# Performance work log

Measured on AMD Instinct MI355X. Metric: run time of the kernel, lower is better.

The kernel has to match this reference:

```python
import jax, jax.numpy as jnp
import numpy as np

B, N, D = 8, 8192, 256
H, DK, M, DH = 8, 32, 64, 512   # heads, per-head key dim, n_omega random features, mlp hidden
DV = D // H                      # per-head value dim
EPS = 1e-3                       # keras LayerNormalization default epsilon


def _layer_norm(x, g, b):
    mu = jnp.mean(x, axis=-1, keepdims=True)
    var = jnp.var(x, axis=-1, keepdims=True)
    return g * (x - mu) * jax.lax.rsqrt(var + EPS) + b


def _phi(x, omega):
    # Performer positive random features. x: (B,H,N,DK), omega: (DK,M)
    x = x / (DK ** 0.25)
    proj = jnp.einsum('bhnd,dm->bhnm', x, omega)
    sq = 0.5 * jnp.sum(x * x, axis=-1, keepdims=True)
    return jnp.exp(proj - sq) / jnp.sqrt(jnp.asarray(M, x.dtype))


def _mhla(x, Wq, bq, Wk, bk, Wv, bv, Wo, bo, omega):
    # x: (B,N,D). Multi-head linear (kernelized) attention.
    q = (x @ Wq + bq).reshape(B, N, H, DK).transpose(0, 2, 1, 3)  # bhnd
    k = (x @ Wk + bk).reshape(B, N, H, DK).transpose(0, 2, 1, 3)
    v = (x @ Wv + bv).reshape(B, N, H, DV).transpose(0, 2, 1, 3)
    pq = _phi(q, omega)                                   # (B,H,N,M)
    pk = _phi(k, omega)                                   # (B,H,N,M)
    kv = jnp.einsum('bhnm,bhnd->bhmd', pk, v)             # (B,H,M,DV)
    num = jnp.einsum('bhnm,bhmd->bhnd', pq, kv)           # (B,H,N,DV)
    den = jnp.einsum('bhnm,bhm->bhn', pq, jnp.sum(pk, axis=2))
    out = num / den[..., None]
    out = out.transpose(0, 2, 1, 3).reshape(B, N, D)
    return out @ Wo + bo


def _gru_gate(x, y, Wr, Ur, Wz, Uz, Wg, Ug, bg):
    # GTrXL gating: x = residual (old state), y = new sublayer output.
    r = jax.nn.sigmoid(y @ Wr + x @ Ur)
    z = jax.nn.sigmoid(y @ Wz + x @ Uz - bg)
    h = jnp.tanh(y @ Wg + (r * x) @ Ug)
    return (1.0 - z) * x + z * h


def setup_inputs() -> dict:
    key = jax.random.key(0)
    ks = iter(jax.random.split(key, 40))
    w = lambda *s: jax.random.normal(next(ks), s, jnp.float32) * 0.02
    inp = {
        'x': jax.random.normal(next(ks), (B, N, D), jnp.float32),
        'ln1_g': jnp.ones((D,), jnp.float32), 'ln1_b': jnp.zeros((D,), jnp.float32),
        'Wq': w(D, H * DK), 'bq': jnp.zeros((H * DK,), jnp.float32),
        'Wk': w(D, H * DK), 'bk': jnp.zeros((H * DK,), jnp.float32),
        'Wv': w(D, H * DV), 'bv': jnp.zeros((H * DV,), jnp.float32),
        'Wo': w(D, D), 'bo': jnp.zeros((D,), jnp.float32),
        'omega': jax.random.normal(next(ks), (DK, M), jnp.float32),
        'g1_Wr': w(D, D), 'g1_Ur': w(D, D), 'g1_Wz': w(D, D), 'g1_Uz': w(D, D),
        'g1_Wg': w(D, D), 'g1_Ug': w(D, D), 'g1_bg': 2.0 * jnp.ones((D,), jnp.float32),
        'ln2_g': jnp.ones((D,), jnp.float32), 'ln2_b': jnp.zeros((D,), jnp.float32),
        'W1': w(D, DH), 'b1': jnp.zeros((DH,), jnp.float32),
        'W2': w(DH, D), 'b2': jnp.zeros((D,), jnp.float32),
        'g2_Wr': w(D, D), 'g2_Ur': w(D, D), 'g2_Wz': w(D, D), 'g2_Uz': w(D, D),
        'g2_Wg': w(D, D), 'g2_Ug': w(D, D), 'g2_bg': 2.0 * jnp.ones((D,), jnp.float32),
    }
    return inp


def reference(x, ln1_g, ln1_b, Wq, bq, Wk, bk, Wv, bv, Wo, bo, omega,
              g1_Wr, g1_Ur, g1_Wz, g1_Uz, g1_Wg, g1_Ug, g1_bg,
              ln2_g, ln2_b, W1, b1, W2, b2,
              g2_Wr, g2_Ur, g2_Wz, g2_Uz, g2_Wg, g2_Ug, g2_bg):
    residual = x
    h = _layer_norm(x, ln1_g, ln1_b)
    h = _mhla(h, Wq, bq, Wk, bk, Wv, bv, Wo, bo, omega)
    h = _gru_gate(residual, h, g1_Wr, g1_Ur, g1_Wz, g1_Uz, g1_Wg, g1_Ug, g1_bg)
    residual = h
    h2 = _layer_norm(h, ln2_g, ln2_b)
    h2 = jax.nn.relu(h2 @ W1 + b1)
    h2 = jax.nn.relu(h2 @ W2 + b2)
    out = _gru_gate(residual, h2, g2_Wr, g2_Ur, g2_Wz, g2_Uz, g2_Wg, g2_Ug, g2_bg)
    return out
```

## Files before the change

kernel.cpp:

```cpp
#include <hip/hip_runtime.h>

#define B_ 8
#define N_ 8192
#define H_ 8
#define KSPLIT 16
#define BN 65536

typedef float f32x4 __attribute__((ext_vector_type(4)));
typedef __bf16 bf16x8 __attribute__((ext_vector_type(8)));
typedef unsigned short u16;

__device__ __forceinline__ u16 f2b(float f) {
  union { float f; unsigned u; } v; v.f = f;
  return (u16)((v.u + 0x7fffu + ((v.u >> 16) & 1u)) >> 16);
}
__device__ __forceinline__ float b2f(u16 u) {
  union { unsigned u; float f; } v; v.u = ((unsigned)u) << 16;
  return v.f;
}

__device__ __forceinline__ void gload16(const void* g, const void* lds) {
  __builtin_amdgcn_global_load_lds(
      (const __attribute__((address_space(1))) unsigned int*)(unsigned long long)g,
      (__attribute__((address_space(3))) unsigned int*)(unsigned long long)lds,
      16, 0, 0);
}

__device__ __forceinline__ void ld16f(const float* p, float* f) {
#pragma unroll
  for (int j = 0; j < 4; ++j) {
    float4 q = *(const float4*)(p + j * 4);
    f[j * 4 + 0] = q.x; f[j * 4 + 1] = q.y; f[j * 4 + 2] = q.z; f[j * 4 + 3] = q.w;
  }
}
__device__ __forceinline__ void ld16b(const u16* p, float* f) {
  uint4 a = *(const uint4*)p, b = *(const uint4*)(p + 8);
  const unsigned uu[8] = {a.x, a.y, a.z, a.w, b.x, b.y, b.z, b.w};
#pragma unroll
  for (int j = 0; j < 8; ++j) {
    f[2 * j]     = b2f((u16)(uu[j] & 0xffff));
    f[2 * j + 1] = b2f((u16)(uu[j] >> 16));
  }
}
__device__ __forceinline__ void st16b(u16* p, const float* f) {
  u16 o[16];
#pragma unroll
  for (int j = 0; j < 16; ++j) o[j] = f2b(f[j]);
  *(uint4*)p = *(const uint4*)o;
  *(uint4*)(p + 8) = *(const uint4*)(o + 8);
}
__device__ __forceinline__ void st16f(float* p, const float* f) {
#pragma unroll
  for (int j = 0; j < 4; ++j) {
    float4 q; q.x = f[j * 4]; q.y = f[j * 4 + 1]; q.z = f[j * 4 + 2]; q.w = f[j * 4 + 3];
    *(float4*)(p + j * 4) = q;
  }
}

template <int MODE, int XBF, int CF32, int BSEL>
__global__ __launch_bounds__(512) void gemm2(
    const u16* __restrict__ A1, int lda1, const u16* __restrict__ A2, int lda2,
    const u16* __restrict__ BT, int ldb,
    const float* __restrict__ bias, const void* __restrict__ auxX,
    const u16* __restrict__ auxZ, const float* __restrict__ auxS,
    void* __restrict__ Cv, void* __restrict__ Cv2, void* __restrict__ Cv3,
    int ldc, int K) {
  __shared__ __align__(16) u16 As[3][4096];
  __shared__ __align__(16) u16 Bs[3][8192];
  const int t = threadIdx.x, lane = t & 63, w = t >> 6;
  const int nwg = gridDim.x * gridDim.y;
  const int flat = blockIdx.x + gridDim.x * blockIdx.y;
  const int wg = (flat & 7) * (nwg >> 3) + (flat >> 3);
  const int bx = wg % gridDim.x, by = wg / gridDim.x;
  const int rowBase = by * 128, colBase = bx * 256;
  const u16* BTb = BSEL ? BT + (size_t)(by >> 6) * 131072 : BT;

  const int lr = lane & 15, kg = lane >> 4;
  const int wrow = (w >> 2) * 64, wcol = (w & 3) * 64;

  f32x4 acc[4][4];
#pragma unroll
  for (int m = 0; m < 4; ++m)
#pragma unroll
    for (int n = 0; n < 4; ++n) acc[m][n] = 0.f;

  const int nt = K >> 5;
  auto stage = [&](int s) {
    const int buf = s % 3;
    const int k0 = s << 5;
    const u16* Ap; int la, ka;
    if (k0 < 256) { Ap = A1; la = lda1; ka = k0; }
    else          { Ap = A2; la = lda2; ka = k0 - 256; }
    {
      int row = t >> 2, sl = t & 3;
      int ks = (sl ^ ((row & 6) >> 1)) * 8;
      gload16(&Ap[(size_t)(rowBase + row) * la + ka + ks], &As[buf][t * 8]);
    }
#pragma unroll
    for (int j = 0; j < 2; ++j) {
      int slot = j * 512 + t;
      int col = slot >> 2, sl = slot & 3;
      int ks = (sl ^ ((col & 6) >> 1)) * 8;
      gload16(&BTb[(size_t)(colBase + col) * ldb + k0 + ks], &Bs[buf][slot * 8]);
    }
  };

  auto lbar = [&]() {
    asm volatile("s_waitcnt lgkmcnt(0)" ::: "memory");
    __builtin_amdgcn_sched_barrier(0);
    __builtin_amdgcn_s_barrier();
    __builtin_amdgcn_sched_barrier(0);
  };

  stage(0);
  stage(1);
  for (int s = 0; s < nt; ++s) {
    const int buf = s % 3;
    if (nt - s > 1) asm volatile("s_waitcnt vmcnt(3)" ::: "memory");
    else            asm volatile("s_waitcnt vmcnt(0)" ::: "memory");
    __builtin_amdgcn_sched_barrier(0);
    __builtin_amdgcn_s_barrier();
    __builtin_amdgcn_sched_barrier(0);
    if (s + 2 < nt) stage(s + 2);
    bf16x8 af[4], bf[4];
#pragma unroll
    for (int m = 0; m < 4; ++m) {
      int row = wrow + m * 16 + lr;
      af[m] = *(const bf16x8*)&As[buf][row * 32 + (kg ^ ((row & 6) >> 1)) * 8];
    }
#pragma unroll
    for (int n = 0; n < 4; ++n) {
      int col = wcol + n * 16 + lr;
      bf[n] = *(const bf16x8*)&Bs[buf][col * 32 + (kg ^ ((col & 6) >> 1)) * 8];
    }
    __builtin_amdgcn_s_setprio(1);
#pragma unroll
    for (int m = 0; m < 4; ++m)
#pragma unroll
      for (int n = 0; n < 4; ++n)
        acc[m][n] = __builtin_amdgcn_mfma_f32_16x16x32_bf16(af[m], bf[n], acc[m][n], 0, 0, 0);
    __builtin_amdgcn_s_setprio(0);
  }

  lbar();
  float* scr = (float*)&Bs[0][0];
#pragma unroll
  for (int m = 0; m < 4; ++m) {
    if (m) lbar();
#pragma unroll
    for (int n = 0; n < 4; ++n)
#pragma unroll
      for (int i = 0; i < 4; ++i)
        scr[((w >> 2) * 16 + kg * 4 + i) * 260 + wcol + n * 16 + lr] = acc[m][n][i];
    lbar();
    const int sr = t >> 4, cs = (t & 15) * 16;
    const int grow = rowBase + (sr >> 4) * 64 + m * 16 + (sr & 15);
    const int gcol = colBase + cs;
    float vv[16];
#pragma unroll
    for (int j = 0; j < 4; ++j) {
      float4 q = *(const float4*)&scr[sr * 260 + cs + j * 4];
      vv[j * 4] = q.x; vv[j * 4 + 1] = q.y; vv[j * 4 + 2] = q.z; vv[j * 4 + 3] = q.w;
    }
    if (MODE == 0 || MODE == 1) {
      float bb[16]; ld16f(&bias[gcol], bb);
#pragma unroll
      for (int j = 0; j < 16; ++j) {
        vv[j] += bb[j];
        if (MODE == 1) vv[j] = fmaxf(vv[j], 0.f);
      }
      st16b(&((u16*)Cv)[(size_t)grow * ldc + gcol], vv);
    } else if (MODE == 5) {
      float sx = auxS[(size_t)grow * 8 + (gcol >> 6)];
#pragma unroll
      for (int j = 0; j < 16; ++j) vv[j] = __expf(vv[j] - sx) * 0.125f;
      st16b(&((u16*)Cv)[(size_t)grow * ldc + gcol], vv);
    } else if (MODE == 6) {
      float sx = auxS[(size_t)grow * 8 + (gcol >> 5)];
#pragma unroll
      for (int j = 0; j < 16; ++j) vv[j] *= sx;
      st16b(&((u16*)Cv)[(size_t)grow * ldc + gcol], vv);
    } else if (MODE == 7) {
      float bb[16]; ld16f(&bias[gcol], bb);
#pragma unroll
      for (int j = 0; j < 16; ++j) vv[j] += bb[j];
      u16* Cp; int c2;
      if (colBase < 256)      { Cp = (u16*)Cv;  c2 = gcol; }
      else if (colBase < 512) { Cp = (u16*)Cv2; c2 = gcol - 256; }
      else                    { Cp = (u16*)Cv3; c2 = gcol - 512; }
      st16b(&Cp[(size_t)grow * ldc + c2], vv);
    } else if (MODE == 8) {
      if (colBase < 256) {
        float xv[16];
        if (XBF) ld16b(&((const u16*)auxX)[(size_t)grow * 256 + gcol], xv);
        else     ld16f(&((const float*)auxX)[(size_t)grow * 256 + gcol], xv);
#pragma unroll
        for (int j = 0; j < 16; ++j) vv[j] = (1.f / (1.f + __expf(-vv[j]))) * xv[j];
        st16b(&((u16*)Cv)[(size_t)grow * ldc + gcol], vv);
      } else {
        float bb[16]; ld16f(&bias[gcol - 256], bb);
#pragma unroll
        for (int j = 0; j < 16; ++j) vv[j] = 1.f / (1.f + __expf(-(vv[j] - bb[j])));
        st16b(&((u16*)Cv2)[(size_t)grow * ldc + gcol - 256], vv);
      }
    } else if (MODE == 4) {
      float zz[16], xv[16];
      ld16b(&auxZ[(size_t)grow * 256 + gcol], zz);
      if (XBF) ld16b(&((const u16*)auxX)[(size_t)grow * 256 + gcol], xv);
      else     ld16f(&((const float*)auxX)[(size_t)grow * 256 + gcol], xv);
#pragma unroll
      for (int j = 0; j < 16; ++j)
        vv[j] = (1.f - zz[j]) * xv[j] + zz[j] * tanhf(vv[j]);
      if (CF32) st16f(&((float*)Cv)[(size_t)grow * ldc + gcol], vv);
      else      st16b(&((u16*)Cv)[(size_t)grow * ldc + gcol], vv);
    }
  }
}

__global__ __launch_bounds__(256) void fkv_kernel(const u16* __restrict__ Kb,
                                                  const u16* __restrict__ Vb,
                                                  const u16* __restrict__ omT,
                                                  float* __restrict__ part) {
  __shared__ __align__(16) char smem[33792];
  u16* Ks  = (u16*)smem;
  u16* omS = Ks + 4096;
  u16* pkT = omS + 2048;
  u16* vT  = pkT + 64 * 72;
  float* sqL = (float*)(vT + 48 * 72);
  float* red = (float*)smem;

  const int bh = blockIdx.x, split = blockIdx.y;
  const int b = bh >> 3, h = bh & 7;
  const int t = threadIdx.x, lane = t & 63, w = t >> 6;
  const int lr = lane & 15, kg = lane >> 4;
  const size_t rbase = (size_t)b * N_ + (size_t)split * (N_ / KSPLIT);

  {
    int m = t >> 2, sl = t & 3;
    gload16(&omT[m * 32 + ((sl ^ ((m & 6) >> 1)) * 8)], &omS[t * 8]);
  }
  for (int i = t; i < 16 * 128; i += 256) {
    int r = 32 + (i >> 7), tok = i & 127;
    vT[r * 72 + tok] = (r == 32) ? (u16)0x3f80 : (u16)0;
  }

  f32x4 kacc[4][3];
#pragma unroll
  for (int mi = 0; mi < 4; ++mi)
#pragma unroll
    for (int ni = 0; ni < 3; ++ni) kacc[mi][ni] = 0.f;

  for (int tile = 0; tile < (N_ / KSPLIT) / 128; ++tile) {
    __syncthreads();
    const size_t gt0 = rbase + tile * 128;
#pragma unroll
    for (int j = 0; j < 2; ++j) {
      int slot = j * 256 + t;
      int tok = slot >> 2, sl = slot & 3;
      gload16(&Kb[(gt0 + tok) * 256 + h * 32 + ((sl ^ ((tok & 6) >> 1)) * 8)],
              &Ks[slot * 8]);
    }
#pragma unroll
    for (int j = 0; j < 2; ++j) {
      int slot = j * 256 + t;
      int tok = slot >> 2, seg = slot & 3;
      uint4 q = *(const uint4*)&Vb[(gt0 + tok) * 256 + h * 32 + seg * 8];
      const unsigned uu[4] = {q.x, q.y, q.z, q.w};
#pragma unroll
      for (int jj = 0; jj < 4; ++jj) {
        vT[(seg * 8 + jj * 2 + 0) * 72 + tok] = (u16)(uu[jj] & 0xffffu);
        vT[(seg * 8 + jj * 2 + 1) * 72 + tok] = (u16)(uu[jj] >> 16);
      }
    }
    asm volatile("s_waitcnt vmcnt(0)" ::: "memory");
    __syncthreads();

    uint4 araw[2];
    bf16x8 af[2];
#pragma unroll
    for (int mi = 0; mi < 2; ++mi) {
      int row = w * 32 + mi * 16 + lr;
      araw[mi] = *(const uint4*)&Ks[row * 32 + (kg ^ ((row & 6) >> 1)) * 8];
      af[mi] = *(const bf16x8*)&araw[mi];
    }
#pragma unroll
    for (int mi = 0; mi < 2; ++mi) {
      const unsigned uu[4] = {araw[mi].x, araw[mi].y, araw[mi].z, araw[mi].w};
      float s = 0.f;
#pragma unroll
      for (int j = 0; j < 4; ++j) {
        float lo = b2f((u16)(uu[j] & 0xffffu)), hi = b2f((u16)(uu[j] >> 16));
        s = __fmaf_rn(lo, lo, s); s = __fmaf_rn(hi, hi, s);
      }
      s += __shfl_xor(s, 16);
      s += __shfl_xor(s, 32);
      if (lane < 16) sqL[w * 32 + mi * 16 + lr] = 0.0883883476483184f * s;
    }
    bf16x8 bo[4];
#pragma unroll
    for (int ni = 0; ni < 4; ++ni) {
      int col = ni * 16 + lr;
      bo[ni] = *(const bf16x8*)&omS[col * 32 + (kg ^ ((col & 6) >> 1)) * 8];
    }
    f32x4 pacc[2][4];
#pragma unroll
    for (int mi = 0; mi < 2; ++mi)
#pragma unroll
      for (int ni = 0; ni < 4; ++ni) {
        f32x4 z = 0.f;
        pacc[mi][ni] = __builtin_amdgcn_mfma_f32_16x16x32_bf16(af[mi], bo[ni], z, 0, 0, 0);
      }
    float sqv[2][4];
#pragma unroll
    for (int mi = 0; mi < 2; ++mi)
#pragma unroll
      for (int i = 0; i < 4; ++i)
        sqv[mi][i] = sqL[w * 32 + mi * 16 + kg * 4 + i];
#pragma unroll
    for (int mi = 0; mi < 2; ++mi)
#pragma unroll
      for (int ni = 0; ni < 4; ++ni) {
        u16 p4[4];
#pragma unroll
        for (int i = 0; i < 4; ++i)
          p4[i] = f2b(__expf(pacc[mi][ni][i] - sqv[mi][i]) * 0.125f);
        int m = ni * 16 + lr;
        int tok = w * 32 + mi * 16 + kg * 4;
        *(unsigned long long*)&pkT[m * 72 + tok] = *(const unsigned long long*)p4;
      }
    __syncthreads();

    {
      int ktok = w * 32;
      bf16x8 a2[4], b2v[3];
#pragma unroll
      for (int mi = 0; mi < 4; ++mi)
        a2[mi] = *(const bf16x8*)&pkT[(mi * 16 + lr) * 72 + ktok + kg * 8];
#pragma unroll
      for (int ni = 0; ni < 3; ++ni)
        b2v[ni] = *(const bf16x8*)&vT[(ni * 16 + lr) * 72 + ktok + kg * 8];
#pragma unroll
      for (int mi = 0; mi < 4; ++mi)
#pragma unroll
        for (int ni = 0; ni < 3; ++ni)
          kacc[mi][ni] = __builtin_amdgcn_mfma_f32_16x16x32_bf16(a2[mi], b2v[ni], kacc[mi][ni], 0, 0, 0);
    }
  }

  __syncthreads();
#pragma unroll
  for (int mi = 0; mi < 4; ++mi) {
#pragma unroll
    for (int ni = 0; ni < 3; ++ni) {
      if (ni < 2) {
#pragma unroll
        for (int i = 0; i < 4; ++i)
          red[w * 2112 + (mi * 16 + kg * 4 + i) * 33 + ni * 16 + lr] = kacc[mi][ni][i];
      } else if (lr == 0) {
#pragma unroll
        for (int i = 0; i < 4; ++i)
          red[w * 2112 + (mi * 16 + kg * 4 + i) * 33 + 32] = kacc[mi][2][i];
      }
    }
  }
  __syncthreads();
  float* dst = part + (size_t)(bh * KSPLIT + split) * 2112;
  for (int idx = t; idx < 2112; idx += 256) {
    int m, c;
    if (idx < 2048) { m = idx >> 5; c = idx & 31; }
    else            { m = idx - 2048; c = 32; }
    float s = 0.f;
#pragma unroll
    for (int w4 = 0; w4 < 4; ++w4) s += red[w4 * 2112 + m * 33 + c];
    dst[idx] = s;
  }
}

struct TJob { const float* s; u16* d; int lds, ldd, rows, cols; };
struct TJobs { TJob j[18]; };
__global__ __launch_bounds__(256) void wt_kernel(TJobs J) {
  TJob jb = J.j[blockIdx.y];
  int ntc = jb.cols >> 6;
  int tile = blockIdx.x;
  if (tile >= (jb.rows >> 6) * ntc) return;
  int tr = (tile / ntc) << 6, tc = (tile % ntc) << 6;
  __shared__ float sm[64][68];
  int t = threadIdx.x;
#pragma unroll
  for (int i = 0; i < 4; ++i) {
    int idx = t + 256 * i;
    int r = idx >> 4, c = (idx & 15) * 4;
    float4 v = *(const float4*)&jb.s[(size_t)(tr + r) * jb.lds + tc + c];
    sm[r][c] = v.x; sm[r][c + 1] = v.y; sm[r][c + 2] = v.z; sm[r][c + 3] = v.w;
  }
  __syncthreads();
#pragma unroll
  for (int i = 0; i < 4; ++i) {
    int idx = t + 256 * i;
    int c = idx >> 4, r = (idx & 15) * 4;
    ushort4 p; p.x = f2b(sm[r][c]); p.y = f2b(sm[r + 1][c]);
    p.z = f2b(sm[r + 2][c]); p.w = f2b(sm[r + 3][c]);
    *(ushort4*)&jb.d[(size_t)(tc + c) * jb.ldd + tr + r] = p;
  }
}

__global__ __launch_bounds__(256) void wphiT_kernel(const float* __restrict__ omega,
                                                    u16* __restrict__ w) {
  int idx = blockIdx.x * 256 + threadIdx.x;
  int c = idx >> 8, k = idx & 255;
  float v = 0.f;
  if ((k >> 5) == (c >> 6)) v = omega[(k & 31) * 64 + (c & 63)] * 0.4204482076268573f;
  w[idx] = f2b(v);
}

__global__ __launch_bounds__(256) void omT_kernel(const float* __restrict__ omega,
                                                  u16* __restrict__ o) {
  int idx = blockIdx.x * 256 + threadIdx.x;
  int m = idx >> 5, k = idx & 31;
  o[idx] = f2b(omega[k * 64 + m] * 0.4204482076268573f);
}

__global__ __launch_bounds__(256) void bias_kernel(const float* bk, const float* bv,
                                                   const float* bq, float* dst) {
  int t = threadIdx.x;
  dst[t] = bk[t]; dst[256 + t] = bv[t]; dst[512 + t] = bq[t];
}

__global__ __launch_bounds__(256) void kvbdT_kernel(const float* __restrict__ kvfin,
                                                    u16* __restrict__ kb) {
  int idx = blockIdx.x * 256 + threadIdx.x;
  int b = idx >> 17, rem = idx & 131071;
  int c = rem >> 9, k = rem & 511;
  float v = 0.f;
  if ((k >> 6) == (c >> 5))
    v = kvfin[(size_t)(b * 8 + (k >> 6)) * 2112 + (k & 63) * 32 + (c & 31)];
  kb[idx] = f2b(v);
}

__global__ __launch_bounds__(256) void cvtb_kernel(const float* __restrict__ x,
                                                   u16* __restrict__ o) {
  size_t i = ((size_t)blockIdx.x * 256 + threadIdx.x) * 16;
  float f[16];
  ld16f(&x[i], f);
  st16b(&o[i], f);
}

template <int XBF>
__global__ __launch_bounds__(256) void ln_kernel2(const void* __restrict__ xv,
                                                  const float* __restrict__ g,
                                                  const float* __restrict__ b,
                                                  u16* __restrict__ out) {
  const int row = blockIdx.x * 4 + (threadIdx.x >> 6);
  const int lane = threadIdx.x & 63;
  float v[4];
  if (XBF) {
    uint2 u = *(const uint2*)&((const u16*)xv)[(size_t)row * 256 + lane * 4];
    v[0] = b2f((u16)(u.x & 0xffff)); v[1] = b2f((u16)(u.x >> 16));
    v[2] = b2f((u16)(u.y & 0xffff)); v[3] = b2f((u16)(u.y >> 16));
  } else {
    float4 f = *(const float4*)&((const float*)xv)[(size_t)row * 256 + lane * 4];
    v[0] = f.x; v[1] = f.y; v[2] = f.z; v[3] = f.w;
  }
  float s = v[0] + v[1] + v[2] + v[3];
  float s2 = v[0] * v[0] + v[1] * v[1] + v[2] * v[2] + v[3] * v[3];
#pragma unroll
  for (int off = 1; off < 64; off <<= 1) {
    s += __shfl_xor(s, off);
    s2 += __shfl_xor(s2, off);
  }
  const float mu = s * (1.f / 256.f);
  const float var = s2 * (1.f / 256.f) - mu * mu;
  const float rs = rsqrtf(var + 1e-3f);
  const float4 gv = *(const float4*)&g[lane * 4];
  const float4 bv = *(const float4*)&b[lane * 4];
  ushort4 o;
  o.x = f2b(gv.x * (v[0] - mu) * rs + bv.x);
  o.y = f2b(gv.y * (v[1] - mu) * rs + bv.y);
  o.z = f2b(gv.z * (v[2] - mu) * rs + bv.z);
  o.w = f2b(gv.w * (v[3] - mu) * rs + bv.w);
  *(ushort4*)&out[(size_t)row * 256 + lane * 4] = o;
}

__global__ __launch_bounds__(256) void sqh_kernel2(const u16* __restrict__ X,
                                                   float* __restrict__ sq) {
  const int row = blockIdx.x * 4 + (threadIdx.x >> 6);
  const int lane = threadIdx.x & 63;
  uint2 u = *(const uint2*)&X[(size_t)row * 256 + lane * 4];
  float a = b2f((u16)(u.x & 0xffff)), bb = b2f((u16)(u.x >> 16));
  float c = b2f((u16)(u.y & 0xffff)), d = b2f((u16)(u.y >> 16));
  float s = a * a + bb * bb + c * c + d * d;
  s += __shfl_xor(s, 1); s += __shfl_xor(s, 2); s += __shfl_xor(s, 4);
  if ((lane & 7) == 0) sq[(size_t)row * 8 + (lane >> 3)] = 0.0883883476483184f * s;
}

__global__ __launch_bounds__(256) void kv_reduce_kernel(const float* __restrict__ part,
                                                        float* __restrict__ fin) {
  const int bh = blockIdx.x, t = threadIdx.x;
  for (int idx = t; idx < 2112; idx += 256) {
    float s = 0.f;
#pragma unroll
    for (int sp = 0; sp < KSPLIT; ++sp) s += part[(size_t)(bh * KSPLIT + sp) * 2112 + idx];
    fin[(size_t)bh * 2112 + idx] = s;
  }
}

__global__ __launch_bounds__(256) void den_kernel(const u16* __restrict__ pq,
                                                  const float* __restrict__ kvfin,
                                                  float* __restrict__ rden) {
  const int row = blockIdx.x * 4 + (threadIdx.x >> 6);
  const int lane = threadIdx.x & 63;
  const int h = lane >> 3, m0 = (lane & 7) * 8;
  const int b = row >> 13;
  const float* s = &kvfin[(size_t)(b * 8 + h) * 2112 + 2048 + m0];
  uint4 pv = *(const uint4*)&pq[(size_t)row * 512 + h * 64 + m0];
  const unsigned uu[4] = {pv.x, pv.y, pv.z, pv.w};
  float acc = 0.f;
#pragma unroll
  for (int j = 0; j < 4; ++j) {
    union { unsigned u; float f; } lo, hi;
    lo.u = uu[j] << 16; hi.u = uu[j] & 0xffff0000u;
    acc = __fmaf_rn(lo.f, s[2 * j], acc);
    acc = __fmaf_rn(hi.f, s[2 * j + 1], acc);
  }
  acc += __shfl_xor(acc, 1); acc += __shfl_xor(acc, 2); acc += __shfl_xor(acc, 4);
  if ((lane & 7) == 0) rden[(size_t)row * 8 + h] = 1.0f / acc;
}

extern "C" void kernel_launch(void* const* d_in, const int* in_sizes, int n_in,
                              void* d_out, int out_size, void* d_ws, size_t ws_size,
                              hipStream_t stream) {
  (void)in_sizes; (void)n_in; (void)out_size; (void)ws_size;
  const float* x     = (const float*)d_in[0];
  const float* ln1_g = (const float*)d_in[1];
  const float* ln1_b = (const float*)d_in[2];
  const float* Wq    = (const float*)d_in[3];
  const float* bq    = (const float*)d_in[4];
  const float* Wk    = (const float*)d_in[5];
  const float* bk    = (const float*)d_in[6];
  const float* Wv    = (const float*)d_in[7];
  const float* bv    = (const float*)d_in[8];
  const float* Wo    = (const float*)d_in[9];
  const float* bo    = (const float*)d_in[10];
  const float* omega = (const float*)d_in[11];
  const float* g1_Wr = (const float*)d_in[12];
  const float* g1_Ur = (const float*)d_in[13];
  const float* g1_Wz = (const float*)d_in[14];
  const float* g1_Uz = (const float*)d_in[15];
  const float* g1_Wg = (const float*)d_in[16];
  const float* g1_Ug = (const float*)d_in[17];
  const float* g1_bg = (const float*)d_in[18];
  const float* ln2_g = (const float*)d_in[19];
  const float* ln2_b = (const float*)d_in[20];
  const float* W1    = (const float*)d_in[21];
  const float* b1    = (const float*)d_in[22];
  const float* W2    = (const float*)d_in[23];
  const float* b2    = (const float*)d_in[24];
  const float* g2_Wr = (const float*)d_in[25];
  const float* g2_Ur = (const float*)d_in[26];
  const float* g2_Wz = (const float*)d_in[27];
  const float* g2_Uz = (const float*)d_in[28];
  const float* g2_Wg = (const float*)d_in[29];
  const float* g2_Ug = (const float*)d_in[30];
  const float* g2_bg = (const float*)d_in[31];

  const size_t SZB = (size_t)BN * 256;
  u16* S0 = (u16*)d_ws;
  u16* S1 = S0 + SZB;
  u16* S2 = S1 + SZB;
  u16* S3 = S2 + SZB;
  u16* qkvT  = S3 + SZB;
  u16* wphiT = qkvT + 768 * 256;
  u16* woT   = wphiT + 512 * 256;
  u16* g1rzT = woT + 65536;
  u16* g1hpT = g1rzT + 262144;
  u16* w1T   = g1hpT + 131072;
  u16* w2T   = w1T + 131072;
  u16* g2rzT = w2T + 131072;
  u16* g2hpT = g2rzT + 262144;
  u16* kvbdT = g2hpT + 131072;
  u16* omTg  = kvbdT + 1048576;
  float* bias768 = (float*)(omTg + 2048);
  float* kvpart  = bias768 + 768;
  float* kvfin   = kvpart + (size_t)64 * KSPLIT * 2112;
  float* sq      = kvfin + 64 * 2112;
  u16* db = (u16*)d_out;
  u16* xb = db + SZB;
  float* outf = (float*)d_out;

  dim3 blk(256), blkG(512);
  dim3 g1c(1, BN / 128), g2c(2, BN / 128), g3c(3, BN / 128);

  TJobs J;
  auto job = [](const float* s, u16* d, int lds, int ldd, int r, int c) {
    TJob t; t.s = s; t.d = d; t.lds = lds; t.ldd = ldd; t.rows = r; t.cols = c; return t;
  };
  J.j[0]  = job(Wk, qkvT, 256, 256, 256, 256);
  J.j[1]  = job(Wv, qkvT + 256 * 256, 256, 256, 256, 256);
  J.j[2]  = job(Wq, qkvT + 512 * 256, 256, 256, 256, 256);
  J.j[3]  = job(Wo, woT, 256, 256, 256, 256);
  J.j[4]  = job(g1_Wr, g1rzT, 256, 512, 256, 256);
  J.j[5]  = job(g1_Ur, g1rzT + 256, 256, 512, 256, 256);
  J.j[6]  = job(g1_Wz, g1rzT + 256 * 512, 256, 512, 256, 256);
  J.j[7]  = job(g1_Uz, g1rzT + 256 * 512 + 256, 256, 512, 256, 256);
  J.j[8]  = job(g1_Wg, g1hpT, 256, 512, 256, 256);
  J.j[9]  = job(g1_Ug, g1hpT + 256, 256, 512, 256, 256);
  J.j[10] = job(W1, w1T, 512, 256, 256, 512);
  J.j[11] = job(W2, w2T, 256, 512, 512, 256);
  J.j[12] = job(g2_Wr, g2rzT, 256, 512, 256, 256);
  J.j[13] = job(g2_Ur, g2rzT + 256, 256, 512, 256, 256);
  J.j[14] = job(g2_Wz, g2rzT + 256 * 512, 256, 512, 256, 256);
  J.j[15] = job(g2_Uz, g2rzT + 256 * 512 + 256, 256, 512, 256, 256);
  J.j[16] = job(g2_Wg, g2hpT, 256, 512, 256, 256);
  J.j[17] = job(g2_Ug, g2hpT + 256, 256, 512, 256, 256);
  wt_kernel<<<dim3(32, 18), blk, 0, stream>>>(J);
  wphiT_kernel<<<512, blk, 0, stream>>>(omega, wphiT);
  omT_kernel<<<8, blk, 0, stream>>>(omega, omTg);
  bias_kernel<<<1, blk, 0, stream>>>(bk, bv, bq, bias768);

  ln_kernel2<0><<<BN / 4, blk, 0, stream>>>(x, ln1_g, ln1_b, S0);
  gemm2<7,0,0,0><<<g3c, blkG, 0, stream>>>(S0, 256, S0, 256, qkvT, 256,
      bias768, nullptr, nullptr, nullptr, S1, S2, S3, 256, 256);
  fkv_kernel<<<dim3(64, KSPLIT), blk, 0, stream>>>(S1, S2, omTg, kvpart);
  kv_reduce_kernel<<<64, blk, 0, stream>>>(kvpart, kvfin);
  kvbdT_kernel<<<4096, blk, 0, stream>>>(kvfin, kvbdT);
  sqh_kernel2<<<BN / 4, blk, 0, stream>>>(S3, sq);
  gemm2<5,0,0,0><<<g2c, blkG, 0, stream>>>(S3, 256, S3, 256, wphiT, 256,
      nullptr, nullptr, nullptr, sq, db, nullptr, nullptr, 512, 256);
  den_kernel<<<BN / 4, blk, 0, stream>>>(db, kvfin, sq);
  gemm2<6,0,0,1><<<g1c, blkG, 0, stream>>>(db, 512, db + 256, 512, kvbdT, 512,
      nullptr, nullptr, nullptr, sq, S3, nullptr, nullptr, 256, 512);
  gemm2<0,0,0,0><<<g1c, blkG, 0, stream>>>(S3, 256, S3, 256, woT, 256,
      bo, nullptr, nullptr, nullptr, db, nullptr, nullptr, 256, 256);
  cvtb_kernel<<<BN / 16, blk, 0, stream>>>(x, xb);
  gemm2<8,0,0,0><<<g2c, blkG, 0, stream>>>(db, 256, xb, 256, g1rzT, 512,
      g1_bg, x, nullptr, nullptr, S1, S2, nullptr, 256, 512);
  gemm2<4,0,0,0><<<g1c, blkG, 0, stream>>>(db, 256, S1, 256, g1hpT, 512,
      nullptr, x, S2, nullptr, S3, nullptr, nullptr, 256, 512);
  ln_kernel2<1><<<BN / 4, blk, 0, stream>>>(S3, ln2_g, ln2_b, S0);
  gemm2<1,0,0,0><<<g2c, blkG, 0, stream>>>(S0, 256, S0, 256, w1T, 256,
      b1, nullptr, nullptr, nullptr, db, nullptr, nullptr, 512, 256);
  gemm2<1,0,0,0><<<g1c, blkG, 0, stream>>>(db, 512, db + 256, 512, w2T, 512,
      b2, nullptr, nullptr, nullptr, S1, nullptr, nullptr, 256, 512);
  gemm2<8,1,0,0><<<g2c, blkG, 0, stream>>>(S1, 256, S3, 256, g2rzT, 512,
      g2_bg, S3, nullptr, nullptr, S2, S0, nullptr, 256, 512);
  gemm2<4,1,1,0><<<g1c, blkG, 0, stream>>>(S1, 256, S2, 256, g2hpT, 512,
      nullptr, S3, S0, nullptr, outf, nullptr, nullptr, 256, 512);
}
```

Measured before the change: 625.6 us.

## Enlarge GEMM row tile to 256 and deepen LDS pipeline to four stages

```diff
diff --git a/kernel.cpp b/kernel.cpp
--- a/kernel.cpp
+++ b/kernel.cpp
@@ -65,43 +65,45 @@
     const u16* __restrict__ auxZ, const float* __restrict__ auxS,
     void* __restrict__ Cv, void* __restrict__ Cv2, void* __restrict__ Cv3,
     int ldc, int K) {
-  __shared__ __align__(16) u16 As[3][4096];
-  __shared__ __align__(16) u16 Bs[3][8192];
+  __shared__ __align__(16) u16 As[4][8192];
+  __shared__ __align__(16) u16 Bs[4][8192];
   const int t = threadIdx.x, lane = t & 63, w = t >> 6;
   const int nwg = gridDim.x * gridDim.y;
   const int flat = blockIdx.x + gridDim.x * blockIdx.y;
   const int wg = (flat & 7) * (nwg >> 3) + (flat >> 3);
   const int bx = wg % gridDim.x, by = wg / gridDim.x;
-  const int rowBase = by * 128, colBase = bx * 256;
-  const u16* BTb = BSEL ? BT + (size_t)(by >> 6) * 131072 : BT;
+  const int rowBase = by * 256, colBase = bx * 256;
+  const u16* BTb = BSEL ? BT + (size_t)(rowBase >> 13) * 131072 : BT;
 
   const int lr = lane & 15, kg = lane >> 4;
-  const int wrow = (w >> 2) * 64, wcol = (w & 3) * 64;
-
-  f32x4 acc[4][4];
-#pragma unroll
-  for (int m = 0; m < 4; ++m)
+  const int wrow = (w >> 2) * 128, wcol = (w & 3) * 64;
+
+  f32x4 acc[8][4];
+#pragma unroll
+  for (int m = 0; m < 8; ++m)
 #pragma unroll
     for (int n = 0; n < 4; ++n) acc[m][n] = 0.f;
 
   const int nt = K >> 5;
   auto stage = [&](int s) {
-    const int buf = s % 3;
+    const int buf = s & 3;
     const int k0 = s << 5;
     const u16* Ap; int la, ka;
     if (k0 < 256) { Ap = A1; la = lda1; ka = k0; }
     else          { Ap = A2; la = lda2; ka = k0 - 256; }
-    {
-      int row = t >> 2, sl = t & 3;
+#pragma unroll
+    for (int j = 0; j < 2; ++j) {
+      int g = j * 512 + t;
+      int row = g >> 2, sl = g & 3;
       int ks = (sl ^ ((row & 6) >> 1)) * 8;
-      gload16(&Ap[(size_t)(rowBase + row) * la + ka + ks], &As[buf][t * 8]);
+      gload16(&Ap[(size_t)(rowBase + row) * la + ka + ks], &As[buf][g * 8]);
     }
 #pragma unroll
     for (int j = 0; j < 2; ++j) {
-      int slot = j * 512 + t;
-      int col = slot >> 2, sl = slot & 3;
+      int g = j * 512 + t;
+      int col = g >> 2, sl = g & 3;
       int ks = (sl ^ ((col & 6) >> 1)) * 8;
-      gload16(&BTb[(size_t)(colBase + col) * ldb + k0 + ks], &Bs[buf][slot * 8]);
+      gload16(&BTb[(size_t)(colBase + col) * ldb + k0 + ks], &Bs[buf][g * 8]);
     }
   };
 
@@ -114,17 +116,20 @@
 
   stage(0);
   stage(1);
+  stage(2);
   for (int s = 0; s < nt; ++s) {
-    const int buf = s % 3;
-    if (nt - s > 1) asm volatile("s_waitcnt vmcnt(3)" ::: "memory");
-    else            asm volatile("s_waitcnt vmcnt(0)" ::: "memory");
+    const int buf = s & 3;
+    const int rem = nt - 1 - s;
+    if (rem >= 2)      asm volatile("s_waitcnt vmcnt(8)" ::: "memory");
+    else if (rem == 1) asm volatile("s_waitcnt vmcnt(4)" ::: "memory");
+    else               asm volatile("s_waitcnt vmcnt(0)" ::: "memory");
     __builtin_amdgcn_sched_barrier(0);
     __builtin_amdgcn_s_barrier();
     __builtin_amdgcn_sched_barrier(0);
-    if (s + 2 < nt) stage(s + 2);
-    bf16x8 af[4], bf[4];
-#pragma unroll
-    for (int m = 0; m < 4; ++m) {
+    if (s + 3 < nt) stage(s + 3);
+    bf16x8 af[8], bf[4];
+#pragma unroll
+    for (int m = 0; m < 8; ++m) {
       int row = wrow + m * 16 + lr;
       af[m] = *(const bf16x8*)&As[buf][row * 32 + (kg ^ ((row & 6) >> 1)) * 8];
     }
@@ -135,7 +140,7 @@
     }
     __builtin_amdgcn_s_setprio(1);
 #pragma unroll
-    for (int m = 0; m < 4; ++m)
+    for (int m = 0; m < 8; ++m)
 #pragma unroll
       for (int n = 0; n < 4; ++n)
         acc[m][n] = __builtin_amdgcn_mfma_f32_16x16x32_bf16(af[m], bf[n], acc[m][n], 0, 0, 0);
@@ -143,18 +148,18 @@
   }
 
   lbar();
-  float* scr = (float*)&Bs[0][0];
-#pragma unroll
-  for (int m = 0; m < 4; ++m) {
-    if (m) lbar();
+  float* scr = (float*)&As[0][0];
+#pragma unroll
+  for (int mf = 0; mf < 8; ++mf) {
+    if (mf) lbar();
 #pragma unroll
     for (int n = 0; n < 4; ++n)
 #pragma unroll
       for (int i = 0; i < 4; ++i)
-        scr[((w >> 2) * 16 + kg * 4 + i) * 260 + wcol + n * 16 + lr] = acc[m][n][i];
+        scr[((w >> 2) * 16 + kg * 4 + i) * 260 + wcol + n * 16 + lr] = acc[mf][n][i];
     lbar();
     const int sr = t >> 4, cs = (t & 15) * 16;
-    const int grow = rowBase + (sr >> 4) * 64 + m * 16 + (sr & 15);
+    const int grow = rowBase + (sr >> 4) * 128 + mf * 16 + (sr & 15);
     const int gcol = colBase + cs;
     float vv[16];
 #pragma unroll
@@ -588,7 +593,7 @@
   float* outf = (float*)d_out;
 
   dim3 blk(256), blkG(512);
-  dim3 g1c(1, BN / 128), g2c(2, BN / 128), g3c(3, BN / 128);
+  dim3 g1c(1, BN / 256), g2c(2, BN / 256), g3c(3, BN / 256);
 
   TJobs J;
   auto job = [](const float* s, u16* d, int lds, int ldd, int r, int c) {
```

Measured after the change: 808.4 us. 29.2% more time.

## Fold Wo into per-batch KV matrix and fuse sq, denominator, LayerNorm into GEMM epilogues

Applied to the files above, without the earlier changes.

```diff
diff --git a/kernel.cpp b/kernel.cpp
--- a/kernel.cpp
+++ b/kernel.cpp
@@ -73,7 +73,10 @@
   const int wg = (flat & 7) * (nwg >> 3) + (flat >> 3);
   const int bx = wg % gridDim.x, by = wg / gridDim.x;
   const int rowBase = by * 128, colBase = bx * 256;
-  const u16* BTb = BSEL ? BT + (size_t)(by >> 6) * 131072 : BT;
+  const int aBase = (BSEL == 2) ? (rowBase & 255) : rowBase;
+  const u16* BTb = BT;
+  if (BSEL == 1) BTb = BT + (size_t)(rowBase >> 13) * 131072;
+  if (BSEL == 2) BTb = BT + (size_t)(rowBase >> 8) * 131072;
 
   const int lr = lane & 15, kg = lane >> 4;
   const int wrow = (w >> 2) * 64, wcol = (w & 3) * 64;
@@ -94,7 +97,7 @@
     {
       int row = t >> 2, sl = t & 3;
       int ks = (sl ^ ((row & 6) >> 1)) * 8;
-      gload16(&Ap[(size_t)(rowBase + row) * la + ka + ks], &As[buf][t * 8]);
+      gload16(&Ap[(size_t)(aBase + row) * la + ka + ks], &As[buf][t * 8]);
     }
 #pragma unroll
     for (int j = 0; j < 2; ++j) {
@@ -175,11 +178,6 @@
 #pragma unroll
       for (int j = 0; j < 16; ++j) vv[j] = __expf(vv[j] - sx) * 0.125f;
       st16b(&((u16*)Cv)[(size_t)grow * ldc + gcol], vv);
-    } else if (MODE == 6) {
-      float sx = auxS[(size_t)grow * 8 + (gcol >> 5)];
-#pragma unroll
-      for (int j = 0; j < 16; ++j) vv[j] *= sx;
-      st16b(&((u16*)Cv)[(size_t)grow * ldc + gcol], vv);
     } else if (MODE == 7) {
       float bb[16]; ld16f(&bias[gcol], bb);
 #pragma unroll
@@ -189,6 +187,15 @@
       else if (colBase < 512) { Cp = (u16*)Cv2; c2 = gcol - 256; }
       else                    { Cp = (u16*)Cv3; c2 = gcol - 512; }
       st16b(&Cp[(size_t)grow * ldc + c2], vv);
+      if (colBase == 512) {
+        float s = 0.f;
+#pragma unroll
+        for (int j = 0; j < 16; ++j) s += vv[j] * vv[j];
+        s += __shfl_xor(s, 1);
+        if ((t & 1) == 0)
+          const_cast<float*>(auxS)[(size_t)grow * 8 + ((gcol - 512) >> 5)] =
+              0.0883883476483184f * s;
+      }
     } else if (MODE == 8) {
       if (colBase < 256) {
         float xv[16];
@@ -213,6 +220,31 @@
         vv[j] = (1.f - zz[j]) * xv[j] + zz[j] * tanhf(vv[j]);
       if (CF32) st16f(&((float*)Cv)[(size_t)grow * ldc + gcol], vv);
       else      st16b(&((u16*)Cv)[(size_t)grow * ldc + gcol], vv);
+    } else if (MODE == 9) {
+      float zz[16], xv[16];
+      ld16b(&auxZ[(size_t)grow * 256 + gcol], zz);
+      ld16b(&((const u16*)auxX)[(size_t)grow * 256 + gcol], xv);
+#pragma unroll
+      for (int j = 0; j < 16; ++j)
+        vv[j] = (1.f - zz[j]) * xv[j] + zz[j] * tanhf(vv[j]);
+      st16b(&((u16*)Cv)[(size_t)grow * 256 + gcol], vv);
+      float s1 = 0.f, s2 = 0.f;
+#pragma unroll
+      for (int j = 0; j < 16; ++j) { s1 += vv[j]; s2 += vv[j] * vv[j]; }
+#pragma unroll
+      for (int off = 1; off < 16; off <<= 1) {
+        s1 += __shfl_xor(s1, off);
+        s2 += __shfl_xor(s2, off);
+      }
+      float mu = s1 * (1.f / 256.f);
+      float var = s2 * (1.f / 256.f) - mu * mu;
+      float rs = rsqrtf(var + 1e-3f);
+      float gg[16], bb2[16];
+      ld16f(&bias[gcol], gg);
+      ld16f(&auxS[gcol], bb2);
+#pragma unroll
+      for (int j = 0; j < 16; ++j) vv[j] = gg[j] * (vv[j] - mu) * rs + bb2[j];
+      st16b(&((u16*)Cv2)[(size_t)grow * 256 + gcol], vv);
     }
   }
 }
@@ -424,16 +456,17 @@
                                                    const float* bq, float* dst) {
   int t = threadIdx.x;
   dst[t] = bk[t]; dst[256 + t] = bv[t]; dst[512 + t] = bq[t];
-}
-
-__global__ __launch_bounds__(256) void kvbdT_kernel(const float* __restrict__ kvfin,
+  dst[768 + t] = 0.f; dst[1024 + t] = 0.f;
+}
+
+__global__ __launch_bounds__(256) void kvbdA_kernel(const float* __restrict__ kvfin,
                                                     u16* __restrict__ kb) {
   int idx = blockIdx.x * 256 + threadIdx.x;
   int b = idx >> 17, rem = idx & 131071;
-  int c = rem >> 9, k = rem & 511;
+  int kp = rem >> 8, d = rem & 255;
   float v = 0.f;
-  if ((k >> 6) == (c >> 5))
-    v = kvfin[(size_t)(b * 8 + (k >> 6)) * 2112 + (k & 63) * 32 + (c & 31)];
+  if ((kp >> 6) == (d >> 5))
+    v = kvfin[(size_t)(b * 8 + (kp >> 6)) * 2112 + (kp & 63) * 32 + (d & 31)];
   kb[idx] = f2b(v);
 }
 
@@ -481,18 +514,6 @@
   *(ushort4*)&out[(size_t)row * 256 + lane * 4] = o;
 }
 
-__global__ __launch_bounds__(256) void sqh_kernel2(const u16* __restrict__ X,
-                                                   float* __restrict__ sq) {
-  const int row = blockIdx.x * 4 + (threadIdx.x >> 6);
-  const int lane = threadIdx.x & 63;
-  uint2 u = *(const uint2*)&X[(size_t)row * 256 + lane * 4];
-  float a = b2f((u16)(u.x & 0xffff)), bb = b2f((u16)(u.x >> 16));
-  float c = b2f((u16)(u.y & 0xffff)), d = b2f((u16)(u.y >> 16));
-  float s = a * a + bb * bb + c * c + d * d;
-  s += __shfl_xor(s, 1); s += __shfl_xor(s, 2); s += __shfl_xor(s, 4);
-  if ((lane & 7) == 0) sq[(size_t)row * 8 + (lane >> 3)] = 0.0883883476483184f * s;
-}
-
 __global__ __launch_bounds__(256) void kv_reduce_kernel(const float* __restrict__ part,
                                                         float* __restrict__ fin) {
   const int bh = blockIdx.x, t = threadIdx.x;
@@ -504,26 +525,31 @@
   }
 }
 
-__global__ __launch_bounds__(256) void den_kernel(const u16* __restrict__ pq,
-                                                  const float* __restrict__ kvfin,
-                                                  float* __restrict__ rden) {
+__global__ __launch_bounds__(256) void den2_kernel(u16* __restrict__ pq,
+                                                   const float* __restrict__ kvfin) {
   const int row = blockIdx.x * 4 + (threadIdx.x >> 6);
   const int lane = threadIdx.x & 63;
   const int h = lane >> 3, m0 = (lane & 7) * 8;
   const int b = row >> 13;
   const float* s = &kvfin[(size_t)(b * 8 + h) * 2112 + 2048 + m0];
-  uint4 pv = *(const uint4*)&pq[(size_t)row * 512 + h * 64 + m0];
+  u16* pp = &pq[(size_t)row * 512 + h * 64 + m0];
+  uint4 pv = *(const uint4*)pp;
   const unsigned uu[4] = {pv.x, pv.y, pv.z, pv.w};
+  float vals[8];
   float acc = 0.f;
 #pragma unroll
   for (int j = 0; j < 4; ++j) {
-    union { unsigned u; float f; } lo, hi;
-    lo.u = uu[j] << 16; hi.u = uu[j] & 0xffff0000u;
-    acc = __fmaf_rn(lo.f, s[2 * j], acc);
-    acc = __fmaf_rn(hi.f, s[2 * j + 1], acc);
+    vals[2 * j]     = b2f((u16)(uu[j] & 0xffffu));
+    vals[2 * j + 1] = b2f((u16)(uu[j] >> 16));
+    acc = __fmaf_rn(vals[2 * j], s[2 * j], acc);
+    acc = __fmaf_rn(vals[2 * j + 1], s[2 * j + 1], acc);
   }
   acc += __shfl_xor(acc, 1); acc += __shfl_xor(acc, 2); acc += __shfl_xor(acc, 4);
-  if ((lane & 7) == 0) rden[(size_t)row * 8 + h] = 1.0f / acc;
+  const float r = 1.0f / acc;
+  u16 o[8];
+#pragma unroll
+  for (int j = 0; j < 8; ++j) o[j] = f2b(vals[j] * r);
+  *(uint4*)pp = *(const uint4*)o;
 }
 
 extern "C" void kernel_launch(void* const* d_in, const int* in_sizes, int n_in,
@@ -577,14 +603,15 @@
   u16* w2T   = w1T + 131072;
   u16* g2rzT = w2T + 131072;
   u16* g2hpT = g2rzT + 262144;
-  u16* kvbdT = g2hpT + 131072;
-  u16* omTg  = kvbdT + 1048576;
+  u16* kvbdA = g2hpT + 131072;
+  u16* WoKVT = kvbdA + 1048576;
+  u16* omTg  = WoKVT + 1048576;
   float* bias768 = (float*)(omTg + 2048);
-  float* kvpart  = bias768 + 768;
+  float* zero512 = bias768 + 768;
+  float* kvpart  = bias768 + 1280;
   float* kvfin   = kvpart + (size_t)64 * KSPLIT * 2112;
-  float* sq      = kvfin + 64 * 2112;
+  float* sqQ     = kvfin + 64 * 2112;
   u16* db = (u16*)d_out;
-  u16* xb = db + SZB;
   float* outf = (float*)d_out;
 
   dim3 blk(256), blkG(512);
@@ -619,24 +646,22 @@
 
   ln_kernel2<0><<<BN / 4, blk, 0, stream>>>(x, ln1_g, ln1_b, S0);
   gemm2<7,0,0,0><<<g3c, blkG, 0, stream>>>(S0, 256, S0, 256, qkvT, 256,
-      bias768, nullptr, nullptr, nullptr, S1, S2, S3, 256, 256);
+      bias768, nullptr, nullptr, sqQ, S1, S2, S3, 256, 256);
   fkv_kernel<<<dim3(64, KSPLIT), blk, 0, stream>>>(S1, S2, omTg, kvpart);
   kv_reduce_kernel<<<64, blk, 0, stream>>>(kvpart, kvfin);
-  kvbdT_kernel<<<4096, blk, 0, stream>>>(kvfin, kvbdT);
-  sqh_kernel2<<<BN / 4, blk, 0, stream>>>(S3, sq);
+  kvbdA_kernel<<<4096, blk, 0, stream>>>(kvfin, kvbdA);
+  gemm2<0,0,0,2><<<dim3(2, 16), blkG, 0, stream>>>(woT, 256, woT, 256, kvbdA, 256,
+      zero512, nullptr, nullptr, nullptr, WoKVT, nullptr, nullptr, 512, 256);
+  cvtb_kernel<<<BN / 16, blk, 0, stream>>>(x, S1);
   gemm2<5,0,0,0><<<g2c, blkG, 0, stream>>>(S3, 256, S3, 256, wphiT, 256,
-      nullptr, nullptr, nullptr, sq, db, nullptr, nullptr, 512, 256);
-  den_kernel<<<BN / 4, blk, 0, stream>>>(db, kvfin, sq);
-  gemm2<6,0,0,1><<<g1c, blkG, 0, stream>>>(db, 512, db + 256, 512, kvbdT, 512,
-      nullptr, nullptr, nullptr, sq, S3, nullptr, nullptr, 256, 512);
-  gemm2<0,0,0,0><<<g1c, blkG, 0, stream>>>(S3, 256, S3, 256, woT, 256,
-      bo, nullptr, nullptr, nullptr, db, nullptr, nullptr, 256, 256);
-  cvtb_kernel<<<BN / 16, blk, 0, stream>>>(x, xb);
-  gemm2<8,0,0,0><<<g2c, blkG, 0, stream>>>(db, 256, xb, 256, g1rzT, 512,
-      g1_bg, x, nullptr, nullptr, S1, S2, nullptr, 256, 512);
-  gemm2<4,0,0,0><<<g1c, blkG, 0, stream>>>(db, 256, S1, 256, g1hpT, 512,
-      nullptr, x, S2, nullptr, S3, nullptr, nullptr, 256, 512);
-  ln_kernel2<1><<<BN / 4, blk, 0, stream>>>(S3, ln2_g, ln2_b, S0);
+      nullptr, nullptr, nullptr, sqQ, db, nullptr, nullptr, 512, 256);
+  den2_kernel<<<BN / 4, blk, 0, stream>>>(db, kvfin);
+  gemm2<0,0,0,1><<<g1c, blkG, 0, stream>>>(db, 512, db + 256, 512, WoKVT, 512,
+      bo, nullptr, nullptr, nullptr, S3, nullptr, nullptr, 256, 512);
+  gemm2<8,1,0,0><<<g2c, blkG, 0, stream>>>(S3, 256, S1, 256, g1rzT, 512,
+      g1_bg, S1, nullptr, nullptr, db, db + SZB, nullptr, 256, 512);
+  gemm2<9,1,0,0><<<g1c, blkG, 0, stream>>>(S3, 256, db, 256, g1hpT, 512,
+      ln2_g, S1, db + SZB, ln2_b, S3, S0, nullptr, 256, 512);
   gemm2<1,0,0,0><<<g2c, blkG, 0, stream>>>(S0, 256, S0, 256, w1T, 256,
       b1, nullptr, nullptr, nullptr, db, nullptr, nullptr, 512, 256);
   gemm2<1,0,0,0><<<g1c, blkG, 0, stream>>>(db, 512, db + 256, 512, w2T, 512,
```

Result: faster. 571.7 us (-8.6%).
